# Performance work log

Measured on AMD Instinct MI355X. Metric: run time of the kernel, lower is better.

## Reference

```python
import jax, jax.numpy as jnp
import numpy as np

B, CIN, COUT, H, W = 16, 128, 128, 64, 64
E, PS, FF = 8, 16, 8
GC, HID, HC = 4 * FF, 64, COUT * 4  # gate_channel, gate hidden, bottleneck hidden


def conv(x, w, stride=1, pad=0, groups=1):
    # x: [B,C,H,W], w: [O,I/groups,kh,kw]
    return jax.lax.conv_general_dilated(
        x, w, (stride, stride), [(pad, pad), (pad, pad)], feature_group_count=groups)


def group_norm(x, scale, bias, groups, eps=1e-5):
    b, c = x.shape[:2]
    xr = x.reshape(b, groups, c // groups, *x.shape[2:])
    m = xr.mean(axis=(2, 3, 4), keepdims=True)
    v = xr.var(axis=(2, 3, 4), keepdims=True)
    xr = (xr - m) * jax.lax.rsqrt(v + eps)
    return xr.reshape(x.shape) * scale[None, :, None, None] + bias[None, :, None, None]


def setup_inputs() -> dict:
    key = jax.random.key(0)
    ks = jax.random.split(key, 8)
    f = lambda k, shp: jax.random.normal(k, shp, jnp.float32) * 0.05
    return dict(
        x=jax.random.normal(ks[0], (B, CIN, H, W), jnp.float32),
        w_exp=f(ks[1], (E, COUT, CIN, 3, 3)),
        gn_exp_s=jnp.ones((E, COUT), jnp.float32),
        gn_exp_b=jnp.zeros((E, COUT), jnp.float32),
        w1=f(ks[2], (GC, HID)), b1=jnp.zeros((HID,), jnp.float32),
        w2=f(ks[3], (HID, E)), b2=jnp.zeros((E,), jnp.float32),
        w_pw1=f(ks[4], (HC, COUT, 1, 1)),
        gn1_s=jnp.ones((HC,), jnp.float32), gn1_b=jnp.zeros((HC,), jnp.float32),
        w_dw=f(ks[5], (HC, 1, 3, 3)),
        gn2_s=jnp.ones((HC,), jnp.float32), gn2_b=jnp.zeros((HC,), jnp.float32),
        w_pw2=f(ks[6], (COUT, HC, 1, 1)),
        gn3_s=jnp.ones((COUT,), jnp.float32), gn3_b=jnp.zeros((COUT,), jnp.float32),
    )


def reference(x, w_exp, gn_exp_s, gn_exp_b, w1, b1, w2, b2,
              w_pw1, gn1_s, gn1_b, w_dw, gn2_s, gn2_b, w_pw2, gn3_s, gn3_b):
    # ---- Conv experts (residual 3x3 conv + GN + SiLU), vmapped over experts ----
    def expert(w, s, b):
        y = conv(x, w, pad=1)
        y = group_norm(y, s, b, groups=min(8, COUT))
        return jax.nn.silu(y) + x  # use_residual=True, CIN == COUT

    ys = jax.vmap(expert)(w_exp, gn_exp_s, gn_exp_b)  # [E,B,C,H,W]

    # ---- Router gate: Fourier features of patch-center coordinates ----
    ph, pw = H // PS, W // PS
    cy = (jnp.arange(ph, dtype=jnp.float32) + 0.5) / ph
    cx = (jnp.arange(pw, dtype=jnp.float32) + 0.5) / pw
    freqs = (2.0 ** jnp.arange(FF, dtype=jnp.float32)) * jnp.pi
    ay = cy[:, None] * freqs  # [ph,FF]
    ax = cx[:, None] * freqs  # [pw,FF]
    feats = jnp.concatenate([
        jnp.broadcast_to(jnp.sin(ay)[:, None, :], (ph, pw, FF)),
        jnp.broadcast_to(jnp.cos(ay)[:, None, :], (ph, pw, FF)),
        jnp.broadcast_to(jnp.sin(ax)[None, :, :], (ph, pw, FF)),
        jnp.broadcast_to(jnp.cos(ax)[None, :, :], (ph, pw, FF)),
    ], axis=-1)  # [ph,pw,4*FF] == gate_channel
    hgate = jax.nn.silu(feats @ w1 + b1)
    wts = jax.nn.softmax(hgate @ w2 + b2, axis=-1)  # [ph,pw,E]

    # ---- Patch-wise combine of expert outputs ----
    wmap = jnp.repeat(jnp.repeat(wts, PS, axis=0), PS, axis=1)  # [H,W,E]
    combined = jnp.einsum('ebchw,hwe->bchw', ys, wmap)

    # ---- Inverted bottleneck: 1x1 -> dw3x3 -> 1x1(stride2) with GN+SiLU ----
    h = jax.nn.silu(group_norm(conv(combined, w_pw1), gn1_s, gn1_b, groups=8))
    h = jax.nn.silu(group_norm(conv(h, w_dw, pad=1, groups=HC), gn2_s, gn2_b, groups=8))
    h = jax.nn.silu(group_norm(conv(h, w_pw2, stride=2), gn3_s, gn3_b, groups=8))
    return h  # [B, COUT, H//2, W//2]
```

## Files before the change

kernel.cpp:

```cpp
#include <hip/hip_runtime.h>
#include <hip/hip_bf16.h>


#define B_ 16
#define CIN_ 128
#define COUT_ 128
#define H_ 64
#define W_ 64
#define HW_ 4096
#define E_ 8
#define FF_ 8
#define GC_ 32
#define HID_ 64
#define HC_ 512

typedef __hip_bfloat16 bf16;
typedef __bf16 bf16x8 __attribute__((ext_vector_type(8)));
typedef float f32x4 __attribute__((ext_vector_type(4)));
typedef float f32x16 __attribute__((ext_vector_type(16)));

__device__ __forceinline__ float siluf(float v) { return v / (1.f + __expf(-v)); }
__device__ __forceinline__ float bf2f(bf16 v) { return __bfloat162float(v); }
__device__ __forceinline__ bf16 f2bf(float v) { return __float2bfloat16(v); }

__device__ __forceinline__ void async16(void* lds, const void* g) {
  __builtin_amdgcn_global_load_lds(
      (const __attribute__((address_space(1))) unsigned int*)g,
      (__attribute__((address_space(3))) unsigned int*)lds, 16, 0, 0);
}

__global__ void gate_kernel(const float* __restrict__ w1, const float* __restrict__ b1,
                            const float* __restrict__ w2, const float* __restrict__ b2,
                            float* __restrict__ wts) {
  int p = threadIdx.x;
  if (p >= 16) return;
  int i = p >> 2, j = p & 3;
  float cy = (i + 0.5f) * 0.25f;
  float cx = (j + 0.5f) * 0.25f;
  float feats[GC_];
#pragma unroll
  for (int f = 0; f < FF_; ++f) {
    float fr = 3.14159265358979f * (float)(1 << f);
    float ay = cy * fr, ax = cx * fr;
    feats[f] = sinf(ay);
    feats[FF_ + f] = cosf(ay);
    feats[2 * FF_ + f] = sinf(ax);
    feats[3 * FF_ + f] = cosf(ax);
  }
  float hid[HID_];
  for (int k = 0; k < HID_; ++k) {
    float a = b1[k];
#pragma unroll
    for (int m = 0; m < GC_; ++m) a = fmaf(feats[m], w1[m * HID_ + k], a);
    hid[k] = siluf(a);
  }
  float lg[E_];
  float mx = -1e30f;
#pragma unroll
  for (int e = 0; e < E_; ++e) {
    float a = b2[e];
    for (int k = 0; k < HID_; ++k) a = fmaf(hid[k], w2[k * E_ + e], a);
    lg[e] = a;
    mx = fmaxf(mx, a);
  }
  float s = 0.f;
#pragma unroll
  for (int e = 0; e < E_; ++e) { lg[e] = __expf(lg[e] - mx); s += lg[e]; }
  float inv = 1.f / s;
#pragma unroll
  for (int e = 0; e < E_; ++e) wts[p * E_ + e] = lg[e] * inv;
}

__global__ __launch_bounds__(256) void xt_kernel(const float* __restrict__ x,
                                                 bf16* __restrict__ xT) {
  __shared__ float t[128][65];
  int b = blockIdx.x >> 6, h = blockIdx.x & 63;
  int tid = threadIdx.x;
  int w = tid & 63, c4 = tid >> 6;
  const float* xb = x + ((size_t)(b * 128) * 64 + h) * 64;
#pragma unroll 4
  for (int rep = 0; rep < 32; ++rep) {
    int ci = rep * 4 + c4;
    t[ci][w] = xb[(size_t)ci * HW_ + w];
  }
  __syncthreads();
  bf16* dst = xT + (size_t)(b * 64 + h) * 8192;
#pragma unroll 4
  for (int rep = 0; rep < 32; ++rep) {
    int o = rep * 256 + tid;
    int cg = o >> 9, w2 = (o >> 3) & 63, lo = o & 7;
    dst[o] = f2bf(t[cg * 8 + lo][w2]);
  }
}

__global__ void wt_kernel(const float* __restrict__ w_exp, bf16* __restrict__ wT) {
  int idx = blockIdx.x * 256 + threadIdx.x;
  if (idx >= 1179648) return;
  int lo = idx & 7;
  int co = (idx >> 3) & 127;
  int cg = (idx >> 10) & 15;
  int rest = idx >> 14;
  int tap = rest % 9, e = rest / 9;
  int ci = cg * 8 + lo;
  wT[idx] = f2bf(w_exp[(((size_t)(e * 128 + co) * 128 + ci) * 9) + tap]);
}

__global__ void wpT_kernel(const float* __restrict__ w_pw1, const float* __restrict__ w_pw2,
                           bf16* __restrict__ wp1T, bf16* __restrict__ wp2T) {
  int idx = blockIdx.x * 256 + threadIdx.x;
  if (idx < 65536) wp1T[idx] = f2bf(w_pw1[idx]);
  else if (idx < 131072) wp2T[idx - 65536] = f2bf(w_pw2[idx - 65536]);
}

__global__ __launch_bounds__(256, 2) void conv_mfma(
    const bf16* __restrict__ xT, const bf16* __restrict__ wT,
    float* __restrict__ statsE, bf16* __restrict__ ys) {
  __shared__ __align__(16) char xls[4 * 6144];
  __shared__ __align__(16) char wls[2][3 * 8192];
  __shared__ float red[4][8][2];

  int blk = blockIdx.x;
  int rt = blk & 15, b = (blk >> 4) & 15, e = blk >> 8;
  int tid = threadIdx.x, lane = tid & 63, wave = tid >> 6;
  int hi = lane >> 5, l31 = lane & 31;
  int h0 = rt * 4;

  f32x16 acc[4][2];
#pragma unroll
  for (int mt = 0; mt < 4; ++mt)
#pragma unroll
    for (int nt = 0; nt < 2; ++nt)
#pragma unroll
      for (int r = 0; r < 16; ++r) acc[mt][nt][r] = 0.f;

  bf16x8 bz;
#pragma unroll
  for (int j = 0; j < 8; ++j) bz[j] = (__bf16)0.f;

  for (int q = 0; q < 4; ++q) {
    if (q) __syncthreads();
    {
      int cg = wave;
#pragma unroll
      for (int r = 0; r < 6; ++r) {
        int h = h0 - 1 + r;
        char* ldst = xls + cg * 6144 + r * 1024;
        if ((unsigned)h < 64u) {
          const char* g = (const char*)xT +
              ((size_t)((b * 64 + h) * 16) + q * 4 + cg) * 1024 + lane * 16;
          async16(ldst, g);
        } else {
          *(uint4*)(ldst + lane * 16) = make_uint4(0u, 0u, 0u, 0u);
        }
      }
    }
#pragma unroll
    for (int s = 0; s < 6; ++s) {
      int seg = wave * 6 + s;
      int tap = seg >> 3, rem = seg & 7;
      int cg = rem >> 1, cb = rem & 1;
      const char* g = (const char*)wT +
          ((size_t)(((e * 9 + tap) * 16) + q * 4 + cg) * 128 + cb * 64) * 16 + lane * 16;
      async16(wls[0] + (tap * 4 + cg) * 2048 + cb * 1024, g);
    }
    __syncthreads();

    for (int dr = 0; dr < 3; ++dr) {
      int buf = dr & 1;
      if (dr < 2) {
#pragma unroll
        for (int s = 0; s < 6; ++s) {
          int seg = wave * 6 + s;
          int tap = seg >> 3, rem = seg & 7;
          int cg = rem >> 1, cb = rem & 1;
          const char* g = (const char*)wT +
              ((size_t)(((e * 9 + (dr + 1) * 3 + tap) * 16) + q * 4 + cg) * 128 + cb * 64) * 16 +
              lane * 16;
          async16(wls[buf ^ 1] + (tap * 4 + cg) * 2048 + cb * 1024, g);
        }
      }
      int r_local = wave + dr;
      const char* wb = wls[buf];
#pragma unroll
      for (int ds = 0; ds < 3; ++ds) {
        const char* wtap = wb + ds * 8192;
#pragma unroll
        for (int ks = 0; ks < 2; ++ks) {
          int cgl = ks * 2 + hi;
          bf16x8 af[4];
#pragma unroll
          for (int mt = 0; mt < 4; ++mt)
            af[mt] = *(const bf16x8*)(wtap + cgl * 2048 + (mt * 32 + l31) * 16);
          bf16x8 bfr[2];
#pragma unroll
          for (int nt = 0; nt < 2; ++nt) {
            int wsrc = nt * 32 + l31 + ds - 1;
            bool valid = (unsigned)wsrc < 64u;
            int wc = valid ? wsrc : 0;
            bf16x8 v = *(const bf16x8*)(xls + cgl * 6144 + (r_local * 64 + wc) * 16);
            bfr[nt] = valid ? v : bz;
          }
#pragma unroll
          for (int mt = 0; mt < 4; ++mt)
#pragma unroll
            for (int nt = 0; nt < 2; ++nt)
              acc[mt][nt] = __builtin_amdgcn_mfma_f32_32x32x16_bf16(
                  af[mt], bfr[nt], acc[mt][nt], 0, 0, 0);
        }
      }
      if (dr < 2) __syncthreads();
    }
  }

  int hh = h0 + wave;
  bf16* yb = ys + (size_t)((e * 16 + b) * 128) * 4096;
#pragma unroll
  for (int mt = 0; mt < 4; ++mt) {
    float s0 = 0.f, ss0 = 0.f, s1 = 0.f, ss1 = 0.f;
#pragma unroll
    for (int nt = 0; nt < 2; ++nt) {
      int w = nt * 32 + l31;
      int pos = hh * 64 + w;
#pragma unroll
      for (int r = 0; r < 16; ++r) {
        float v = acc[mt][nt][r];
        if (r < 8) { s0 += v; ss0 += v * v; } else { s1 += v; ss1 += v * v; }
        int row = (r & 3) + 8 * (r >> 2) + 4 * hi;
        yb[(size_t)(mt * 32 + row) * 4096 + pos] = f2bf(v);
      }
    }
#pragma unroll
    for (int off = 32; off; off >>= 1) {
      s0 += __shfl_down(s0, off, 64);
      ss0 += __shfl_down(ss0, off, 64);
      s1 += __shfl_down(s1, off, 64);
      ss1 += __shfl_down(ss1, off, 64);
    }
    if (lane == 0) {
      red[wave][mt * 2][0] = s0; red[wave][mt * 2][1] = ss0;
      red[wave][mt * 2 + 1][0] = s1; red[wave][mt * 2 + 1][1] = ss1;
    }
  }
  __syncthreads();
  if (tid < 16) {
    int g = tid >> 1, which = tid & 1;
    float t = red[0][g][which] + red[1][g][which] + red[2][g][which] + red[3][g][which];
    atomicAdd(&statsE[((e * 16 + b) * 8 + g) * 2 + which], t);
  }
}

__global__ void finalize_stats(float* __restrict__ st, int n, float inv) {
  int i = blockIdx.x * 256 + threadIdx.x;
  if (i >= n) return;
  float S = st[i * 2], SS = st[i * 2 + 1];
  float mean = S * inv;
  float var = SS * inv - mean * mean;
  st[i * 2] = mean;
  st[i * 2 + 1] = rsqrtf(var + 1e-5f);
}

__global__ __launch_bounds__(256) void combine_cl(
    const float* __restrict__ x, const bf16* __restrict__ ys,
    const float* __restrict__ st, const float* __restrict__ gns,
    const float* __restrict__ gnb, const float* __restrict__ wts,
    bf16* __restrict__ ccl) {
  __shared__ bf16 tile[64][132];
  int b = blockIdx.x >> 6, h = blockIdx.x & 63;
  int t = threadIdx.x;
  int w32 = t & 31, coq = t >> 5;
  float m_[8], r_[8];
#pragma unroll
  for (int e = 0; e < 8; ++e) {
    m_[e] = st[((e * 16 + b) * 8 + coq) * 2];
    r_[e] = st[((e * 16 + b) * 8 + coq) * 2 + 1];
  }
#pragma unroll
  for (int wt2 = 0; wt2 < 2; ++wt2) {
    int w = wt2 * 32 + w32;
    int pid = (h >> 4) * 4 + (w >> 4);
    int pos = h * 64 + w;
    float wt_[8];
#pragma unroll
    for (int e = 0; e < 8; ++e) wt_[e] = wts[pid * 8 + e];
    for (int coi = 0; coi < 16; ++coi) {
      int co = coq * 16 + coi;
      float v = x[((size_t)(b * 128 + co) << 12) + pos];
#pragma unroll
      for (int e = 0; e < 8; ++e) {
        float y = bf2f(ys[((size_t)((e * 16 + b) * 128 + co) << 12) + pos]);
        float yn = (y - m_[e]) * r_[e] * gns[e * 128 + co] + gnb[e * 128 + co];
        v += siluf(yn) * wt_[e];
      }
      tile[w][co] = f2bf(v);
    }
  }
  __syncthreads();
  int row = t >> 2, q = t & 3;
  char* dst = (char*)ccl + ((size_t)(b * 4096 + h * 64 + row)) * 256 + q * 64;
  const char* src = (const char*)&tile[row][0] + q * 64;
#pragma unroll
  for (int i = 0; i < 4; ++i)
    *(uint4*)(dst + i * 16) = *(const uint4*)(src + i * 16);
}

__global__ __launch_bounds__(256) void pw1_mfma(
    const bf16* __restrict__ ccl, const bf16* __restrict__ wp1T,
    bf16* __restrict__ h1cl, float* __restrict__ stats1) {
  __shared__ __align__(16) char ls[65536];
  __shared__ float red[4][2][2];
  char* als = ls;
  char* bls = ls + 32768;
  int blk = blockIdx.x;
  int ntile = blk & 511, mtile = blk >> 9;
  int n0 = ntile * 128, m0 = mtile * 128;
  int t = threadIdx.x, lane = t & 63, wave = t >> 6;
  int quad = lane >> 4, l15 = lane & 15;
  int b = n0 >> 12;

#pragma unroll
  for (int i = 0; i < 8; ++i) {
    int id = t + 256 * i;
    int r = id >> 4, c = id & 15;
    *(uint4*)(als + c * 2048 + r * 16) =
        *(const uint4*)((const char*)wp1T + (size_t)(m0 + r) * 256 + c * 16);
    *(uint4*)(bls + c * 2048 + r * 16) =
        *(const uint4*)((const char*)ccl + (size_t)(n0 + r) * 256 + c * 16);
  }
  __syncthreads();

  f32x4 acc[8][2];
#pragma unroll
  for (int mt = 0; mt < 8; ++mt)
#pragma unroll
    for (int nt = 0; nt < 2; ++nt) acc[mt][nt] = (f32x4){0.f, 0.f, 0.f, 0.f};

#pragma unroll
  for (int kc = 0; kc < 4; ++kc) {
    int cgq = kc * 4 + quad;
    bf16x8 af[8];
#pragma unroll
    for (int mt = 0; mt < 8; ++mt)
      af[mt] = *(const bf16x8*)(als + cgq * 2048 + (mt * 16 + l15) * 16);
    bf16x8 bfr[2];
#pragma unroll
    for (int nt = 0; nt < 2; ++nt)
      bfr[nt] = *(const bf16x8*)(bls + cgq * 2048 + (wave * 32 + nt * 16 + l15) * 16);
#pragma unroll
    for (int mt = 0; mt < 8; ++mt)
#pragma unroll
      for (int nt = 0; nt < 2; ++nt)
        acc[mt][nt] = __builtin_amdgcn_mfma_f32_16x16x32_bf16(
            af[mt], bfr[nt], acc[mt][nt], 0, 0, 0);
  }

  __syncthreads();
  float s[2] = {0.f, 0.f}, ss[2] = {0.f, 0.f};
  bf16* tile = (bf16*)ls;
#pragma unroll
  for (int mt = 0; mt < 8; ++mt) {
    int gi = mt >> 2;
#pragma unroll
    for (int nt = 0; nt < 2; ++nt) {
      int n = wave * 32 + nt * 16 + l15;
#pragma unroll
      for (int r = 0; r < 4; ++r) {
        float v = acc[mt][nt][r];
        s[gi] += v;
        ss[gi] += v * v;
        tile[n * 132 + mt * 16 + quad * 4 + r] = f2bf(v);
      }
    }
  }
#pragma unroll
  for (int gi = 0; gi < 2; ++gi) {
#pragma unroll
    for (int off = 32; off; off >>= 1) {
      s[gi] += __shfl_down(s[gi], off, 64);
      ss[gi] += __shfl_down(ss[gi], off, 64);
    }
  }
  if (lane == 0) {
    red[wave][0][0] = s[0]; red[wave][0][1] = ss[0];
    red[wave][1][0] = s[1]; red[wave][1][1] = ss[1];
  }
  __syncthreads();
  if (t < 4) {
    int gi = t >> 1, which = t & 1;
    float v = red[0][gi][which] + red[1][gi][which] + red[2][gi][which] + red[3][gi][which];
    atomicAdd(&stats1[(b * 8 + mtile * 2 + gi) * 2 + which], v);
  }
#pragma unroll
  for (int i = 0; i < 8; ++i) {
    int id = t + 256 * i;
    int r = id >> 4, q = id & 15;
    char* dst = (char*)h1cl + (size_t)(n0 + r) * 1024 + m0 * 2 + q * 16;
    const char* src = (const char*)tile + r * 264 + q * 16;
    *(uint4*)dst = *(const uint4*)src;
  }
}

__global__ __launch_bounds__(256) void dw_cl(
    const bf16* __restrict__ h1cl, const float* __restrict__ w_dw,
    const float* __restrict__ st1, const float* __restrict__ gs,
    const float* __restrict__ gb, bf16* __restrict__ h2cl,
    float* __restrict__ stats2) {
  __shared__ __align__(16) bf16 tile[18 * 66 * 16];
  __shared__ float red2[4][2];
  int blk = blockIdx.x;
  int ht = blk & 3, hcg = (blk >> 2) & 31, b = blk >> 7;
  int h0 = ht * 16;
  int hc0 = hcg * 16;
  int hcb = hcg >> 2;
  int t = threadIdx.x;

  float mean = st1[(b * 8 + hcb) * 2], rstd = st1[(b * 8 + hcb) * 2 + 1];
  float scale[16], shift[16];
#pragma unroll
  for (int j = 0; j < 16; ++j) {
    float g = gs[hc0 + j];
    scale[j] = rstd * g;
    shift[j] = gb[hc0 + j] - mean * rstd * g;
  }

  for (int i = 0; i < 5; ++i) {
    int idx = t + 256 * i;
    if (idx >= 1188) break;
    int row = idx / 66, wslot = idx - row * 66;
    int hh = h0 - 1 + row;
    int w = wslot - 1;
    int swz = (wslot >> 2) & 3;
    bf16* dst = tile + (row * 66 + wslot) * 16;
    if ((unsigned)hh < 64u && (unsigned)w < 64u) {
      const char* p = (const char*)h1cl + ((size_t)(b * 4096 + hh * 64 + w) * 512 + hc0) * 2;
      uint4 a0 = *(const uint4*)p;
      uint4 a1 = *(const uint4*)(p + 16);
      const bf16* pv = (const bf16*)&a0;
      const bf16* pv1 = (const bf16*)&a1;
      bf16 outv[16];
#pragma unroll
      for (int j = 0; j < 8; ++j)
        outv[j] = f2bf(siluf(bf2f(pv[j]) * scale[j] + shift[j]));
#pragma unroll
      for (int j = 0; j < 8; ++j)
        outv[8 + j] = f2bf(siluf(bf2f(pv1[j]) * scale[8 + j] + shift[8 + j]));
#pragma unroll
      for (int qq = 0; qq < 4; ++qq) {
        int ph = (qq + swz) & 3;
        *(uint2*)(dst + ph * 4) = *(const uint2*)(outv + qq * 4);
      }
    } else {
      *(uint4*)dst = make_uint4(0u, 0u, 0u, 0u);
      *(uint4*)(dst + 8) = make_uint4(0u, 0u, 0u, 0u);
    }
  }
  __syncthreads();

  int w = t & 63, q = t >> 6;
  float wv[9][4];
#pragma unroll
  for (int j = 0; j < 4; ++j) {
    int hc = hc0 + q * 4 + j;
#pragma unroll
    for (int tap = 0; tap < 9; ++tap) wv[tap][j] = w_dw[hc * 9 + tap];
  }

  f32x4 win[3][3];
  float acc_s = 0.f, acc_ss = 0.f;

  auto ld4 = [&](int r, int dwi) -> f32x4 {
    int slot = w + dwi;
    int ph = (q + (slot >> 2)) & 3;
    const bf16* p = tile + (r * 66 + slot) * 16 + ph * 4;
    uint2 u = *(const uint2*)p;
    const bf16* pb = (const bf16*)&u;
    return (f32x4){bf2f(pb[0]), bf2f(pb[1]), bf2f(pb[2]), bf2f(pb[3])};
  };

#pragma unroll
  for (int dwi = 0; dwi < 3; ++dwi) {
    win[0][dwi] = ld4(0, dwi);
    win[1][dwi] = ld4(1, dwi);
  }
#pragma unroll
  for (int orow = 0; orow < 16; ++orow) {
    int rnew = orow + 2;
    int ringn = rnew % 3;
#pragma unroll
    for (int dwi = 0; dwi < 3; ++dwi) win[ringn][dwi] = ld4(rnew, dwi);
    f32x4 acc = (f32x4){0.f, 0.f, 0.f, 0.f};
#pragma unroll
    for (int dr = 0; dr < 3; ++dr) {
      int ring = (orow + dr) % 3;
#pragma unroll
      for (int dwi = 0; dwi < 3; ++dwi) {
#pragma unroll
        for (int j = 0; j < 4; ++j)
          acc[j] = fmaf(win[ring][dwi][j], wv[dr * 3 + dwi][j], acc[j]);
      }
    }
#pragma unroll
    for (int j = 0; j < 4; ++j) { acc_s += acc[j]; acc_ss += acc[j] * acc[j]; }
    if (!(orow & 1) && !(w & 1)) {
      int hglob = h0 + orow;
      int pos2 = (hglob >> 1) * 32 + (w >> 1);
      bf16 tmp[4];
#pragma unroll
      for (int j = 0; j < 4; ++j) tmp[j] = f2bf(acc[j]);
      *(uint2*)((char*)h2cl + ((size_t)(b * 1024 + pos2) * 512 + hc0 + q * 4) * 2) =
          *(const uint2*)tmp;
    }
  }

#pragma unroll
  for (int off = 32; off; off >>= 1) {
    acc_s += __shfl_down(acc_s, off, 64);
    acc_ss += __shfl_down(acc_ss, off, 64);
  }
  int wave = t >> 6;
  if ((t & 63) == 0) { red2[wave][0] = acc_s; red2[wave][1] = acc_ss; }
  __syncthreads();
  if (t < 2) {
    float v = red2[0][t] + red2[1][t] + red2[2][t] + red2[3][t];
    atomicAdd(&stats2[(b * 8 + hcb) * 2 + t], v);
  }
}

__global__ void norm2_kernel(bf16* __restrict__ h2, const float* __restrict__ st2,
                             const float* __restrict__ gs, const float* __restrict__ gb) {
  int tg = blockIdx.x * 256 + threadIdx.x;
  int e8 = tg * 8;
  int hc0 = e8 & 511;
  int rest = e8 >> 9;
  int bq = rest >> 10;
  int g = hc0 >> 6;
  float mean = st2[(bq * 8 + g) * 2], rstd = st2[(bq * 8 + g) * 2 + 1];
  uint4 v = *(const uint4*)((const char*)h2 + (size_t)tg * 16);
  bf16* pv = (bf16*)&v;
  bf16 outv[8];
#pragma unroll
  for (int j = 0; j < 8; ++j) {
    float x = bf2f(pv[j]);
    x = (x - mean) * rstd * gs[hc0 + j] + gb[hc0 + j];
    outv[j] = f2bf(siluf(x));
  }
  *(uint4*)((char*)h2 + (size_t)tg * 16) = *(const uint4*)outv;
}

__global__ __launch_bounds__(256) void pw2_mfma(
    const bf16* __restrict__ h2n, const bf16* __restrict__ wp2T,
    float* __restrict__ h3, float* __restrict__ stats3) {
  __shared__ __align__(16) char als[2][8192];
  __shared__ __align__(16) char bls[2][4096];
  __shared__ float red[4][8][2];
  int blk = blockIdx.x;
  int n0 = blk * 64;
  int b = n0 >> 10, posb = n0 & 1023;
  int t = threadIdx.x, lane = t & 63, wave = t >> 6;
  int quad = lane >> 4, l15 = lane & 15;
  int wbase = wave * 16;

  f32x4 acc[8];
#pragma unroll
  for (int mt = 0; mt < 8; ++mt) acc[mt] = (f32x4){0.f, 0.f, 0.f, 0.f};

  {
#pragma unroll
    for (int i = 0; i < 2; ++i) {
      int id = t + 256 * i;
      int c4 = id >> 7, r = id & 127;
      *(uint4*)(als[0] + c4 * 2048 + r * 16) =
          *(const uint4*)((const char*)wp2T + (size_t)r * 1024 + c4 * 16);
    }
    int c4 = t >> 6, r = t & 63;
    *(uint4*)(bls[0] + c4 * 1024 + r * 16) =
        *(const uint4*)((const char*)h2n + (size_t)(n0 + r) * 1024 + c4 * 16);
  }
  for (int kc = 0; kc < 16; ++kc) {
    __syncthreads();
    if (kc + 1 < 16) {
      int nb = (kc + 1) & 1;
#pragma unroll
      for (int i = 0; i < 2; ++i) {
        int id = t + 256 * i;
        int c4 = id >> 7, r = id & 127;
        *(uint4*)(als[nb] + c4 * 2048 + r * 16) =
            *(const uint4*)((const char*)wp2T + (size_t)r * 1024 + ((kc + 1) * 4 + c4) * 16);
      }
      int c4 = t >> 6, r = t & 63;
      *(uint4*)(bls[nb] + c4 * 1024 + r * 16) =
          *(const uint4*)((const char*)h2n + (size_t)(n0 + r) * 1024 + ((kc + 1) * 4 + c4) * 16);
    }
    int buf = kc & 1;
    bf16x8 bf1 = *(const bf16x8*)(bls[buf] + quad * 1024 + (wbase + l15) * 16);
#pragma unroll
    for (int mt = 0; mt < 8; ++mt) {
      bf16x8 af = *(const bf16x8*)(als[buf] + quad * 2048 + (mt * 16 + l15) * 16);
      acc[mt] = __builtin_amdgcn_mfma_f32_16x16x32_bf16(af, bf1, acc[mt], 0, 0, 0);
    }
  }

#pragma unroll
  for (int mt = 0; mt < 8; ++mt) {
    float s = 0.f, ss = 0.f;
    int pos = posb + wbase + l15;
#pragma unroll
    for (int r = 0; r < 4; ++r) {
      float v = acc[mt][r];
      s += v;
      ss += v * v;
      int co = mt * 16 + quad * 4 + r;
      h3[(size_t)(b * 128 + co) * 1024 + pos] = v;
    }
#pragma unroll
    for (int off = 32; off; off >>= 1) {
      s += __shfl_down(s, off, 64);
      ss += __shfl_down(ss, off, 64);
    }
    if (lane == 0) { red[wave][mt][0] = s; red[wave][mt][1] = ss; }
  }
  __syncthreads();
  if (t < 16) {
    int mt = t >> 1, which = t & 1;
    float v = red[0][mt][which] + red[1][mt][which] + red[2][mt][which] + red[3][mt][which];
    atomicAdd(&stats3[(b * 8 + mt) * 2 + which], v);
  }
}

__global__ void out_kernel(const float* __restrict__ h3, const float* __restrict__ stats,
                           const float* __restrict__ gs, const float* __restrict__ gb,
                           float* __restrict__ out) {
  const int total = B_ * COUT_ * 1024;
  for (int idx = blockIdx.x * blockDim.x + threadIdx.x; idx < total; idx += gridDim.x * blockDim.x) {
    int c = (idx >> 10) & 127;
    int b = idx >> 17;
    int bg = b * 8 + (c >> 4);
    float S = stats[bg * 2], SS = stats[bg * 2 + 1];
    float mean = S * (1.f / 16384.f);
    float var = SS * (1.f / 16384.f) - mean * mean;
    float rstd = rsqrtf(var + 1e-5f);
    float v = (h3[idx] - mean) * rstd * gs[c] + gb[c];
    out[idx] = siluf(v);
  }
}

extern "C" void kernel_launch(void* const* d_in, const int* in_sizes, int n_in,
                              void* d_out, int out_size, void* d_ws, size_t ws_size,
                              hipStream_t stream) {
  const float* x = (const float*)d_in[0];
  const float* w_exp = (const float*)d_in[1];
  const float* gn_exp_s = (const float*)d_in[2];
  const float* gn_exp_b = (const float*)d_in[3];
  const float* w1 = (const float*)d_in[4];
  const float* b1 = (const float*)d_in[5];
  const float* w2 = (const float*)d_in[6];
  const float* b2 = (const float*)d_in[7];
  const float* w_pw1 = (const float*)d_in[8];
  const float* gn1_s = (const float*)d_in[9];
  const float* gn1_b = (const float*)d_in[10];
  const float* w_dw = (const float*)d_in[11];
  const float* gn2_s = (const float*)d_in[12];
  const float* gn2_b = (const float*)d_in[13];
  const float* w_pw2 = (const float*)d_in[14];
  const float* gn3_s = (const float*)d_in[15];
  const float* gn3_b = (const float*)d_in[16];

  char* ws = (char*)d_ws;
  const size_t WP1T_OFF = 16384;
  const size_t WP2T_OFF = WP1T_OFF + 131072;
  const size_t XT_OFF = WP2T_OFF + 131072;
  const size_t WT_OFF = XT_OFF + 16777216;
  const size_t YS_OFF = WT_OFF + 2359296;
  const size_t NEEDED = YS_OFF + 134217728;
  if (ws_size < NEEDED) return;

  float* wts = (float*)ws;
  float* stats1 = (float*)(ws + 1024);
  float* stats2 = (float*)(ws + 2048);
  float* stats3 = (float*)(ws + 3072);
  float* statsE = (float*)(ws + 4096);
  bf16* wp1T = (bf16*)(ws + WP1T_OFF);
  bf16* wp2T = (bf16*)(ws + WP2T_OFF);
  bf16* xT = (bf16*)(ws + XT_OFF);
  bf16* ccl = (bf16*)(ws + XT_OFF);
  bf16* wT = (bf16*)(ws + WT_OFF);
  bf16* ys = (bf16*)(ws + YS_OFF);
  bf16* h1cl = (bf16*)(ws + YS_OFF);
  bf16* h2cl = (bf16*)(ws + YS_OFF + 67108864);
  float* h3 = (float*)(ws + YS_OFF + 83886080);

  hipMemsetAsync(ws, 0, 16384, stream);
  gate_kernel<<<1, 64, 0, stream>>>(w1, b1, w2, b2, wts);
  xt_kernel<<<B_ * 64, 256, 0, stream>>>(x, xT);
  wt_kernel<<<4608, 256, 0, stream>>>(w_exp, wT);
  wpT_kernel<<<512, 256, 0, stream>>>(w_pw1, w_pw2, wp1T, wp2T);
  conv_mfma<<<E_ * B_ * 16, 256, 0, stream>>>(xT, wT, statsE, ys);
  finalize_stats<<<4, 256, 0, stream>>>(statsE, 1024, 1.f / 65536.f);
  combine_cl<<<B_ * 64, 256, 0, stream>>>(x, ys, statsE, gn_exp_s, gn_exp_b, wts, ccl);
  pw1_mfma<<<4 * 512, 256, 0, stream>>>(ccl, wp1T, h1cl, stats1);
  finalize_stats<<<1, 128, 0, stream>>>(stats1, 128, 1.f / 262144.f);
  dw_cl<<<B_ * 32 * 4, 256, 0, stream>>>(h1cl, w_dw, stats1, gn1_s, gn1_b, h2cl, stats2);
  finalize_stats<<<1, 128, 0, stream>>>(stats2, 128, 1.f / 262144.f);
  norm2_kernel<<<4096, 256, 0, stream>>>(h2cl, stats2, gn2_s, gn2_b);
  pw2_mfma<<<256, 256, 0, stream>>>(h2cl, wp2T, h3, stats3);
  out_kernel<<<1024, 256, 0, stream>>>(h3, stats3, gn3_s, gn3_b, (float*)d_out);
}
```

Before: 491.9 us.

## Pad conv input tile with zero halo, remap blocks per XCD, software-pipeline MFMA operand loads

The LDS input tile gains a zero halo column on each side, and the out-of-range top/bottom rows are zeroed once per block. This removes the per-load boundary checks and selects in the inner loop. The block index is remapped so each XCD handles two fixed batch images, which should improve L2 locality of input reads. The MFMA loop is flattened into 12 steps with double-buffered register prefetch of A/B fragments to overlap LDS reads with MFMA issue, at the cost of extra registers and slightly more LDS.

```diff
diff --git a/kernel.cpp b/kernel.cpp
--- a/kernel.cpp
+++ b/kernel.cpp
@@ -115,16 +115,32 @@
 __global__ __launch_bounds__(256, 2) void conv_mfma(
     const bf16* __restrict__ xT, const bf16* __restrict__ wT,
     float* __restrict__ statsE, bf16* __restrict__ ys) {
-  __shared__ __align__(16) char xls[4 * 6144];
+  __shared__ __align__(16) char xls[4 * 6336];
   __shared__ __align__(16) char wls[2][3 * 8192];
   __shared__ float red[4][8][2];
 
   int blk = blockIdx.x;
-  int rt = blk & 15, b = (blk >> 4) & 15, e = blk >> 8;
+  int xcd = blk & 7;
+  int r2 = blk >> 3;
+  int b = xcd * 2 + (r2 & 1);
+  int rest = r2 >> 1;
+  int rt = rest & 15, e = rest >> 4;
+
   int tid = threadIdx.x, lane = tid & 63, wave = tid >> 6;
   int hi = lane >> 5, l31 = lane & 31;
   int h0 = rt * 4;
 
+  if (tid < 48) {
+    int cg = tid / 12, rem = tid % 12;
+    int r = rem >> 1, edge = rem & 1;
+    *(uint4*)(xls + cg * 6336 + r * 1056 + edge * 1040) = make_uint4(0u, 0u, 0u, 0u);
+  }
+  int rbad = (rt == 0) ? 0 : (rt == 15 ? 5 : -1);
+  if (rbad >= 0) {
+    int cg = tid >> 6, slot = (tid & 63) + 1;
+    *(uint4*)(xls + cg * 6336 + rbad * 1056 + slot * 16) = make_uint4(0u, 0u, 0u, 0u);
+  }
+
   f32x16 acc[4][2];
 #pragma unroll
   for (int mt = 0; mt < 4; ++mt)
@@ -132,10 +148,6 @@
     for (int nt = 0; nt < 2; ++nt)
 #pragma unroll
       for (int r = 0; r < 16; ++r) acc[mt][nt][r] = 0.f;
-
-  bf16x8 bz;
-#pragma unroll
-  for (int j = 0; j < 8; ++j) bz[j] = (__bf16)0.f;
 
   for (int q = 0; q < 4; ++q) {
     if (q) __syncthreads();
@@ -144,13 +156,10 @@
 #pragma unroll
       for (int r = 0; r < 6; ++r) {
         int h = h0 - 1 + r;
-        char* ldst = xls + cg * 6144 + r * 1024;
         if ((unsigned)h < 64u) {
           const char* g = (const char*)xT +
               ((size_t)((b * 64 + h) * 16) + q * 4 + cg) * 1024 + lane * 16;
-          async16(ldst, g);
-        } else {
-          *(uint4*)(ldst + lane * 16) = make_uint4(0u, 0u, 0u, 0u);
+          async16(xls + cg * 6336 + r * 1056 + 16, g);
         }
       }
     }
@@ -181,32 +190,39 @@
       }
       int r_local = wave + dr;
       const char* wb = wls[buf];
-#pragma unroll
-      for (int ds = 0; ds < 3; ++ds) {
-        const char* wtap = wb + ds * 8192;
-#pragma unroll
-        for (int ks = 0; ks < 2; ++ks) {
-          int cgl = ks * 2 + hi;
-          bf16x8 af[4];
-#pragma unroll
-          for (int mt = 0; mt < 4; ++mt)
-            af[mt] = *(const bf16x8*)(wtap + cgl * 2048 + (mt * 32 + l31) * 16);
-          bf16x8 bfr[2];
-#pragma unroll
-          for (int nt = 0; nt < 2; ++nt) {
-            int wsrc = nt * 32 + l31 + ds - 1;
-            bool valid = (unsigned)wsrc < 64u;
-            int wc = valid ? wsrc : 0;
-            bf16x8 v = *(const bf16x8*)(xls + cgl * 6144 + (r_local * 64 + wc) * 16);
-            bfr[nt] = valid ? v : bz;
+      const char* xrow = xls;
+      bf16x8 afp[2][2], bfp[2][2];
+      {
+        int cgl = hi;
+        afp[0][0] = *(const bf16x8*)(wb + cgl * 2048 + (0 * 32 + l31) * 16);
+        afp[0][1] = *(const bf16x8*)(wb + cgl * 2048 + (1 * 32 + l31) * 16);
+        const char* xr = xrow + cgl * 6336 + r_local * 1056;
+        bfp[0][0] = *(const bf16x8*)(xr + (0 * 32 + l31 + 0) * 16);
+        bfp[0][1] = *(const bf16x8*)(xr + (1 * 32 + l31 + 0) * 16);
+      }
+#pragma unroll
+      for (int s = 0; s < 12; ++s) {
+        int mh = s & 1;
+        int cura = s & 1, curb = (s >> 1) & 1;
+        if (s < 11) {
+          int s1 = s + 1;
+          int ds1 = s1 >> 2, ks1 = (s1 >> 1) & 1, mh1 = s1 & 1;
+          int cgl1 = ks1 * 2 + hi;
+          const char* wt1 = wb + ds1 * 8192 + cgl1 * 2048;
+          afp[s1 & 1][0] = *(const bf16x8*)(wt1 + ((mh1 * 2 + 0) * 32 + l31) * 16);
+          afp[s1 & 1][1] = *(const bf16x8*)(wt1 + ((mh1 * 2 + 1) * 32 + l31) * 16);
+          if (mh1 == 0) {
+            const char* xr1 = xrow + cgl1 * 6336 + r_local * 1056;
+            bfp[(s1 >> 1) & 1][0] = *(const bf16x8*)(xr1 + (0 * 32 + l31 + ds1) * 16);
+            bfp[(s1 >> 1) & 1][1] = *(const bf16x8*)(xr1 + (1 * 32 + l31 + ds1) * 16);
           }
-#pragma unroll
-          for (int mt = 0; mt < 4; ++mt)
-#pragma unroll
-            for (int nt = 0; nt < 2; ++nt)
-              acc[mt][nt] = __builtin_amdgcn_mfma_f32_32x32x16_bf16(
-                  af[mt], bfr[nt], acc[mt][nt], 0, 0, 0);
         }
+#pragma unroll
+        for (int i = 0; i < 2; ++i)
+#pragma unroll
+          for (int nt = 0; nt < 2; ++nt)
+            acc[mh * 2 + i][nt] = __builtin_amdgcn_mfma_f32_32x32x16_bf16(
+                afp[cura][i], bfp[curb][nt], acc[mh * 2 + i][nt], 0, 0, 0);
       }
       if (dr < 2) __syncthreads();
     }
```

Result: no change. 484.1 us (-1.6%).
